# Kernel optimization log

Hardware: AMD Instinct MI355X
Metric: run time of the kernel (lower is better)

## Reference

```python
import jax, jax.numpy as jnp
import numpy as np

EMBED_NUM = 50000
EMBED_DIM = 300
HIDDEN = 512          # per-direction GRU hidden
ATT = 256             # attention_size
LABELS = 3
B, S = 64, 256
MAX_NORM = 5.0        # embedding max_norm


def _gru_dir(xw, Whh, bhh, hidden):
    """Run a single-direction GRU. xw: precomputed input proj [B,S,3H]."""
    def step(h, xt):
        gh = h @ Whh.T + bhh                      # [B,3H]
        xr, xz, xn = jnp.split(xt, 3, axis=-1)
        hr, hz, hn = jnp.split(gh, 3, axis=-1)
        r = jax.nn.sigmoid(xr + hr)
        z = jax.nn.sigmoid(xz + hz)
        n = jnp.tanh(xn + r * hn)
        h = (1.0 - z) * n + z * h
        return h, h
    h0 = jnp.zeros((xw.shape[0], hidden), dtype=xw.dtype)
    _, hs = jax.lax.scan(step, h0, jnp.swapaxes(xw, 0, 1))  # [S,B,H]
    return jnp.swapaxes(hs, 0, 1)                            # [B,S,H]


def setup_inputs() -> dict:
    key = jax.random.key(0)
    ks = jax.random.split(key, 20)
    x = jax.random.randint(ks[0], (B, S), 0, EMBED_NUM)
    target_start = jax.random.randint(ks[1], (B,), 0, S - 32)
    span = jax.random.randint(ks[2], (B,), 0, 20)
    target_end = jnp.minimum(target_start + span, S - 1)

    def rn(k, shape, fan_in):
        return jax.random.normal(k, shape, dtype=jnp.float32) * (1.0 / np.sqrt(fan_in))

    return {
        "x": x, "target_start": target_start, "target_end": target_end,
        "emb": jax.random.normal(ks[3], (EMBED_NUM, EMBED_DIM), dtype=jnp.float32) * 0.1,
        "Wih_f": rn(ks[4], (3 * HIDDEN, EMBED_DIM), EMBED_DIM),
        "Whh_f": rn(ks[5], (3 * HIDDEN, HIDDEN), HIDDEN),
        "bih_f": jnp.zeros((3 * HIDDEN,), jnp.float32),
        "bhh_f": jnp.zeros((3 * HIDDEN,), jnp.float32),
        "Wih_b": rn(ks[6], (3 * HIDDEN, EMBED_DIM), EMBED_DIM),
        "Whh_b": rn(ks[7], (3 * HIDDEN, HIDDEN), HIDDEN),
        "bih_b": jnp.zeros((3 * HIDDEN,), jnp.float32),
        "bhh_b": jnp.zeros((3 * HIDDEN,), jnp.float32),
        "W1": rn(ks[8], (ATT, 4 * HIDDEN), 4 * HIDDEN),
        "b1": jnp.zeros((ATT,), jnp.float32),
        "u": rn(ks[9], (ATT, ATT), ATT),
        "W2": rn(ks[10], (LABELS, 2 * HIDDEN), 2 * HIDDEN),
        "b2": jnp.zeros((LABELS,), jnp.float32),
    }


def reference(x, target_start, target_end, emb, Wih_f, Whh_f, bih_f, bhh_f,
              Wih_b, Whh_b, bih_b, bhh_b, W1, b1, u, W2, b2):
    # Embedding lookup with max_norm renorm (p=2), dropout = identity (eval)
    e = emb[x]                                                   # [B,S,E]
    nrm = jnp.linalg.norm(e, axis=-1, keepdims=True)
    e = e * jnp.minimum(1.0, MAX_NORM / (nrm + 1e-7))

    # Bidirectional GRU
    h_f = _gru_dir(e @ Wih_f.T + bih_f, Whh_f, bhh_f, HIDDEN)
    xb = e[:, ::-1, :]
    h_b = _gru_dir(xb @ Wih_b.T + bih_b, Whh_b, bhh_b, HIDDEN)[:, ::-1, :]
    h = jnp.concatenate([h_f, h_b], axis=-1)                     # [B,S,2H]

    # Ragged span mean-pool (vectorized replacement of the python loop)
    t = jnp.arange(S)
    mask = (t[None, :] >= target_start[:, None]) & (t[None, :] <= target_end[:, None])
    cnt = (target_end - target_start + 1).astype(h.dtype)        # [B]
    target = (h * mask[..., None].astype(h.dtype)).sum(axis=1) / cnt[:, None]  # [B,2H]

    # Concat each timestep hidden with its batch's target vector
    cat = jnp.concatenate([h, jnp.broadcast_to(target[:, None, :], h.shape)], axis=-1)  # [B,S,4H]
    o = jnp.tanh(cat @ W1.T + b1)                                # [B,S,A]

    # Per-batch attention scoring: beta[b] = u @ o[b]^T  -> [B,A,S]
    beta = jnp.einsum("ka,bsa->bks", u, o)
    alfa = jax.nn.softmax(beta, axis=-1)                         # softmax over sequence
    result = jnp.einsum("bks,bsh->bkh", alfa, h)                 # [B,A,2H]
    return result @ W2.T + b2                                    # [B,A,LABELS]
```

## Files before the change

### kernel.cpp

```cpp
#include <hip/hip_runtime.h>
#include <math.h>

#define BB   64
#define SS   256
#define ED   300
#define EDP  304
#define HH   512
#define G3   1536
#define ATT_ 256
#define BS_  16384
#define CHK  64
#define NCHK 4

__global__ void k_embed(const int* __restrict__ x, const float* __restrict__ emb,
                        float* __restrict__ e) {
    int row = blockIdx.x;
    int tok = x[row];
    const float* src = emb + (size_t)tok * ED;
    float* dst = e + (size_t)row * EDP;
    int tid = threadIdx.x;
    float v[3];
    float ss = 0.f;
#pragma unroll
    for (int i = 0; i < 3; ++i) {
        int k = tid + i * 128;
        float t = (k < ED) ? src[k] : 0.f;
        v[i] = t;
        ss += t * t;
    }
    for (int off = 32; off > 0; off >>= 1) ss += __shfl_xor(ss, off, 64);
    __shared__ float red[2];
    if ((tid & 63) == 0) red[tid >> 6] = ss;
    __syncthreads();
    float nrm = sqrtf(red[0] + red[1]);
    float scale = fminf(1.0f, 5.0f / (nrm + 1e-7f));
#pragma unroll
    for (int i = 0; i < 3; ++i) {
        int k = tid + i * 128;
        if (k < EDP) dst[k] = (k < ED) ? v[i] * scale : 0.f;
    }
}

#define PN0 933888
#define PN1 (PN0 + 3072)
#define PN2 (PN1 + 262144)
#define PN3 (PN2 + 1572864)

__global__ void k_prep_all(const float* __restrict__ Wihf, const float* __restrict__ Wihb,
                           const float* __restrict__ bihf, const float* __restrict__ bihb,
                           const float* __restrict__ W1,
                           const float* __restrict__ Whhf, const float* __restrict__ Whhb,
                           float* __restrict__ Wtc, float* __restrict__ bcc,
                           float* __restrict__ W1at, float* __restrict__ Wq) {
    int idx = blockIdx.x * blockDim.x + threadIdx.x;
    int stride = gridDim.x * blockDim.x;
    for (int i = idx; i < PN3; i += stride) {
        if (i < PN0) {
            int k = i / 3072, n = i - k * 3072;
            int dir = n >= 1536, nn = n - dir * 1536;
            const float* Wih = dir ? Wihb : Wihf;
            Wtc[i] = (k < ED) ? Wih[(size_t)nn * ED + k] : 0.f;
        } else if (i < PN1) {
            int j = i - PN0;
            bcc[j] = (j < 1536) ? bihf[j] : bihb[j - 1536];
        } else if (i < PN2) {
            int j = i - PN1;
            int n = j >> 10, k = j & 1023;
            W1at[(size_t)k * ATT_ + n] = W1[(size_t)n * 2048 + k];
        } else {
            int j = i - PN2;
            int dir = j / 786432, jj = j - dir * 786432;
            const float* Whh = dir ? Whhb : Whhf;
            int oc  = jj / 98304;
            int rem = jj - oc * 98304;
            int m   = rem / 3072;
            int r2  = rem - m * 3072;
            int t   = r2 >> 2;
            int e   = r2 & 3;
            int r   = t >> 2;
            int ks  = t & 3;
            int g   = r >> 6;
            int ul  = r & 63;
            int u   = oc * 64 + ul;
            int kq  = (oc * 16 + ks + 4 * m) & 127;
            Wq[j] = Whh[((size_t)(g * 512 + u)) * 512 + kq * 4 + e];
        }
    }
}

#define BSKEW(n) ((n) + (((n) >> 5) << 2))

template <int KT, int EPI>
__global__ void __launch_bounds__(256) k_gemm128(
    const float* __restrict__ A, int lda, long strideA,
    const float* __restrict__ Bm, int ldb, long strideB,
    float* __restrict__ C, int ldc, long strideC,
    int M, int N, int K,
    const float* __restrict__ bias, const float* __restrict__ bias2,
    int spos0, int spos1) {
    __shared__ float As[KT * 132];
    __shared__ float Bs[KT * 144];
    const int tid = threadIdx.x;
    const int tx = tid & 15, ty = tid >> 4;
    const int mbase = blockIdx.y * 128, nbase = blockIdx.x * 128;
    const int spos = (spos0 >= 0 && nbase >= 1536) ? spos1 : spos0;
    const float* Ab = A + (long)blockIdx.z * strideA;
    const float* Bb = Bm + (long)blockIdx.z * strideB;
    float* Cb = C + (long)blockIdx.z * strideC;
    float acc[8][8] = {};
    const int bgrp = tx * 8 + ((tx >> 2) << 2);
    for (int k0 = 0; k0 < K; k0 += KT) {
#pragma unroll
        for (int t = 0; t < 2; ++t) {
            int f = tid * 2 + t;
            int r = f >> 2, c4 = f & 3;
            int row = mbase + r;
            int arow = (spos >= 0) ? ((row >> 6) * 256 + spos + (row & 63)) : row;
            float4 a = *(const float4*)&Ab[(size_t)arow * lda + k0 + c4 * 4];
            As[(c4 * 4 + 0) * 132 + r] = a.x;
            As[(c4 * 4 + 1) * 132 + r] = a.y;
            As[(c4 * 4 + 2) * 132 + r] = a.z;
            As[(c4 * 4 + 3) * 132 + r] = a.w;
        }
#pragma unroll
        for (int t = 0; t < 2; ++t) {
            int f = tid * 2 + t;
            int kk = f >> 5, n = (f & 31) * 4;
            float4 b = *(const float4*)&Bb[(size_t)(k0 + kk) * ldb + nbase + n];
            *(float4*)&Bs[kk * 144 + BSKEW(n)] = b;
        }
        __syncthreads();
#pragma unroll
        for (int kk = 0; kk < KT; ++kk) {
            const float4* pa = (const float4*)&As[kk * 132 + ty * 8];
            float4 a0 = pa[0], a1 = pa[1];
            const float4* pb = (const float4*)&Bs[kk * 144 + bgrp];
            float4 b0 = pb[0], b1 = pb[1];
            float av[8] = {a0.x, a0.y, a0.z, a0.w, a1.x, a1.y, a1.z, a1.w};
            float bv[8] = {b0.x, b0.y, b0.z, b0.w, b1.x, b1.y, b1.z, b1.w};
#pragma unroll
            for (int i = 0; i < 8; ++i)
#pragma unroll
                for (int j = 0; j < 8; ++j) acc[i][j] += av[i] * bv[j];
        }
        __syncthreads();
    }
    if (EPI == 3) {
        const int row0 = mbase + ty * 8;
        const size_t bb = (size_t)(row0 >> 8) * strideC;
#pragma unroll
        for (int j = 0; j < 8; ++j) {
            int col = nbase + tx * 8 + j;
            float vj[8];
#pragma unroll
            for (int i = 0; i < 8; ++i) {
                int row = row0 + i;
                vj[i] = tanhf(acc[i][j] + bias2[(size_t)(row >> 8) * ATT_ + col]);
            }
            float* cp = &Cb[bb + (size_t)col * ldc + (row0 & 255)];
            ((float4*)cp)[0] = make_float4(vj[0], vj[1], vj[2], vj[3]);
            ((float4*)cp)[1] = make_float4(vj[4], vj[5], vj[6], vj[7]);
        }
    } else {
#pragma unroll
        for (int i = 0; i < 8; ++i) {
            int row = mbase + ty * 8 + i;
            float vout[8];
#pragma unroll
            for (int j = 0; j < 8; ++j) {
                int col = nbase + tx * 8 + j;
                float v = acc[i][j];
                if (EPI == 1) v += bias[col];
                if (EPI == 2) v = tanhf(v + bias2[(size_t)(row >> 8) * ATT_ + col]);
                vout[j] = v;
            }
            float4* cp = (float4*)&Cb[(size_t)row * ldc + nbase + tx * 8];
            cp[0] = make_float4(vout[0], vout[1], vout[2], vout[3]);
            cp[1] = make_float4(vout[4], vout[5], vout[6], vout[7]);
        }
    }
}

__device__ __forceinline__ float sigmoidf_(float v) { return 1.f / (1.f + expf(-v)); }

#define GRU_FMA4(mm)                                                        \
    {                                                                       \
        float4 h0 = hs4[kq];                                                \
        float4 h1 = hs4[128 + kq];                                          \
        float4 h2 = hs4[256 + kq];                                          \
        float4 h3 = hs4[384 + kq];                                          \
        float4 w = wp[(size_t)(mm) * 768];                                  \
        acc0 += h0.x * w.x + h0.y * w.y + h0.z * w.z + h0.w * w.w;          \
        acc1 += h1.x * w.x + h1.y * w.y + h1.z * w.z + h1.w * w.w;          \
        acc2 += h2.x * w.x + h2.y * w.y + h2.z * w.z + h2.w * w.w;          \
        acc3 += h3.x * w.x + h3.y * w.y + h3.z * w.z + h3.w * w.w;          \
        kq = (kq + 4) & 127;                                                \
    }

__global__ void __launch_bounds__(768)
k_gru_oct(const float* __restrict__ xw,
          const float* __restrict__ Wq,
          const float* __restrict__ bhhf, const float* __restrict__ bhhb,
          float* __restrict__ h_all,
          float* __restrict__ hx,
          unsigned* __restrict__ flg,
          int c) {
    const int bid   = blockIdx.x;
    const int group = bid >> 4;
    const int dir   = (bid >> 3) & 1;
    const int oc    = bid & 7;
    const int tid   = threadIdx.x;
    const float* __restrict__ bhh = dir ? bhhb : bhhf;
    const float4* __restrict__ wp =
        (const float4*)Wq + (size_t)(dir * 8 + oc) * 24576 + tid;
    __shared__ __align__(16) float hs[2048];
    __shared__ float gact[768];

    if (c == 0) {
        for (int t = tid; t < 2048; t += 768) hs[t] = 0.f;
    } else {
        const int prevpos = dir ? (256 - CHK * c) : (CHK * c - 1);
        for (int t = tid; t < 2048; t += 768) {
            int bb = t >> 9, uu = t & 511;
            hs[t] = h_all[((size_t)(group * 4 + bb) * 256 + prevpos) * 1024 +
                          dir * 512 + uu];
        }
    }
    const int ks  = tid & 3;
    const int r   = tid >> 2;
    const int bbg = tid >> 6;
    const int ulg = tid & 63;
    const int ug  = oc * 64 + ulg;
    float b0 = 0.f, b1 = 0.f, b2 = 0.f;
    if (tid < 256) { b0 = bhh[ug]; b1 = bhh[512 + ug]; b2 = bhh[1024 + ug]; }
    const int fbase = (dir * 16 + group) * 8;
    const int fi = (fbase + oc) * 32;
    __syncthreads();
    const float4* __restrict__ hs4 = (const float4*)hs;

    for (int j = 0; j < CHK; ++j) {
        const int gi  = c * CHK + j;
        const int pos = dir ? (255 - gi) : gi;
        float ph0 = 0.f, ph1 = 0.f, ph2 = 0.f;
        if (j > 0) {
            if (tid < 7) {
                const unsigned* f = &flg[(fbase + ((oc + 1 + tid) & 7)) * 32];
                while (__hip_atomic_load(f, __ATOMIC_RELAXED,
                                         __HIP_MEMORY_SCOPE_AGENT) < (unsigned)gi)
                    __builtin_amdgcn_s_sleep(1);
            }
            __syncthreads();
            const float* hxb = hx + (((size_t)((gi - 1) & 1) * 2 + dir) * 16 +
                                     group) * 2048;
            {
                int i0 = tid;
                int bb = i0 / 448, pi = i0 - bb * 448;
                int pu = pi + ((pi >= oc * 64) ? 64 : 0);
                ph0 = __hip_atomic_load(&hxb[bb * 512 + pu], __ATOMIC_RELAXED,
                                        __HIP_MEMORY_SCOPE_AGENT);
                int i1 = tid + 768;
                bb = i1 / 448; pi = i1 - bb * 448;
                pu = pi + ((pi >= oc * 64) ? 64 : 0);
                ph1 = __hip_atomic_load(&hxb[bb * 512 + pu], __ATOMIC_RELAXED,
                                        __HIP_MEMORY_SCOPE_AGENT);
                if (tid < 256) {
                    int i2 = tid + 1536;
                    bb = i2 / 448; pi = i2 - bb * 448;
                    pu = pi + ((pi >= oc * 64) ? 64 : 0);
                    ph2 = __hip_atomic_load(&hxb[bb * 512 + pu], __ATOMIC_RELAXED,
                                            __HIP_MEMORY_SCOPE_AGENT);
                }
            }
        }
        float xr = 0.f, xz = 0.f, xn = 0.f;
        if (tid < 256) {
            const int b = group * 4 + bbg;
            const int crow = b * CHK + (dir ? (CHK - 1 - j) : j);
            const float* __restrict__ xrow = xw + (size_t)crow * 3072 + dir * 1536;
            xr = xrow[ug]; xz = xrow[512 + ug]; xn = xrow[1024 + ug];
        }
        if (gi > 0) {
            float acc0 = 0.f, acc1 = 0.f, acc2 = 0.f, acc3 = 0.f;
            int kq = oc * 16 + ks;
            if (j > 0) {
#pragma unroll
                for (int m = 0; m < 4; ++m) GRU_FMA4(m);
                {
                    int i0 = tid;
                    int bb = i0 / 448, pi = i0 - bb * 448;
                    int pu = pi + ((pi >= oc * 64) ? 64 : 0);
                    hs[bb * 512 + pu] = ph0;
                    int i1 = tid + 768;
                    bb = i1 / 448; pi = i1 - bb * 448;
                    pu = pi + ((pi >= oc * 64) ? 64 : 0);
                    hs[bb * 512 + pu] = ph1;
                    if (tid < 256) {
                        int i2 = tid + 1536;
                        bb = i2 / 448; pi = i2 - bb * 448;
                        pu = pi + ((pi >= oc * 64) ? 64 : 0);
                        hs[bb * 512 + pu] = ph2;
                    }
                }
                __syncthreads();
#pragma unroll 4
                for (int m = 4; m < 32; ++m) GRU_FMA4(m);
            } else {
#pragma unroll 4
                for (int m = 0; m < 32; ++m) GRU_FMA4(m);
            }
            acc0 += __shfl_xor(acc0, 1, 64); acc0 += __shfl_xor(acc0, 2, 64);
            acc1 += __shfl_xor(acc1, 1, 64); acc1 += __shfl_xor(acc1, 2, 64);
            acc2 += __shfl_xor(acc2, 1, 64); acc2 += __shfl_xor(acc2, 2, 64);
            acc3 += __shfl_xor(acc3, 1, 64); acc3 += __shfl_xor(acc3, 2, 64);
            if (ks == 0) {
                gact[r] = acc0;
                gact[192 + r] = acc1;
                gact[384 + r] = acc2;
                gact[576 + r] = acc3;
            }
        }
        __syncthreads();
        if (tid < 256) {
            float hr = (gi > 0) ? gact[bbg * 192 + ulg] : 0.f;
            float hz = (gi > 0) ? gact[bbg * 192 + 64 + ulg] : 0.f;
            float hn = (gi > 0) ? gact[bbg * 192 + 128 + ulg] : 0.f;
            float rr = sigmoidf_(xr + b0 + hr);
            float zz = sigmoidf_(xz + b1 + hz);
            float nn = tanhf(xn + rr * (b2 + hn));
            float h = (1.f - zz) * nn + zz * hs[bbg * 512 + ug];
            hs[bbg * 512 + ug] = h;
            const int b = group * 4 + bbg;
            __hip_atomic_store(&h_all[((size_t)b * 256 + pos) * 1024 +
                                      dir * 512 + ug],
                               h, __ATOMIC_RELAXED, __HIP_MEMORY_SCOPE_AGENT);
            __hip_atomic_store(&hx[(((size_t)(gi & 1) * 2 + dir) * 16 + group) *
                                       2048 + bbg * 512 + ug],
                               h, __ATOMIC_RELAXED, __HIP_MEMORY_SCOPE_AGENT);
        }
        __syncthreads();
        if (tid == 0)
            __hip_atomic_store(&flg[fi], (unsigned)(gi + 1), __ATOMIC_RELEASE,
                               __HIP_MEMORY_SCOPE_AGENT);
    }
}

__global__ void k_target_tmp2(const float* __restrict__ h_all,
                              const int* __restrict__ ts, const int* __restrict__ te,
                              const float* __restrict__ W1, const float* __restrict__ b1,
                              float* __restrict__ tmp2) {
    int b = blockIdx.x;
    int tid = threadIdx.x;
    __shared__ __align__(16) float tg[1024];
    int s0 = ts[b], s1 = te[b];
    float inv = 1.f / (float)(s1 - s0 + 1);
    for (int d = tid; d < 1024; d += 256) {
        float acc = 0.f;
        for (int s = s0; s <= s1; ++s) acc += h_all[((size_t)b * 256 + s) * 1024 + d];
        tg[d] = acc * inv;
    }
    __syncthreads();
    const float4* wrow = (const float4*)(W1 + (size_t)tid * 2048 + 1024);
    const float4* tg4 = (const float4*)tg;
    float acc = b1[tid];
    for (int k = 0; k < 256; ++k) {
        float4 w = wrow[k], t = tg4[k];
        acc += w.x * t.x + w.y * t.y + w.z * t.z + w.w * t.w;
    }
    tmp2[(size_t)b * ATT_ + tid] = acc;
}

__global__ void k_softmax(float* __restrict__ beta) {
    int row = blockIdx.x;
    float* p = beta + (size_t)row * 256;
    int tid = threadIdx.x;
    float v = p[tid];
    float m = v;
    for (int off = 32; off > 0; off >>= 1) m = fmaxf(m, __shfl_xor(m, off, 64));
    __shared__ float red[4];
    if ((tid & 63) == 0) red[tid >> 6] = m;
    __syncthreads();
    m = fmaxf(fmaxf(red[0], red[1]), fmaxf(red[2], red[3]));
    float e = expf(v - m);
    float ssum = e;
    for (int off = 32; off > 0; off >>= 1) ssum += __shfl_xor(ssum, off, 64);
    __shared__ float red2[4];
    if ((tid & 63) == 0) red2[tid >> 6] = ssum;
    __syncthreads();
    float tot = red2[0] + red2[1] + red2[2] + red2[3];
    p[tid] = e / tot;
}

__global__ void k_final(const float* __restrict__ result, const float* __restrict__ W2,
                        const float* __restrict__ b2, float* __restrict__ out) {
    int row = blockIdx.x;
    int tid = threadIdx.x;
    const float* r = result + (size_t)row * 1024;
    float a0 = 0.f, a1 = 0.f, a2 = 0.f;
    for (int h = tid; h < 1024; h += 256) {
        float rv = r[h];
        a0 += rv * W2[h];
        a1 += rv * W2[1024 + h];
        a2 += rv * W2[2048 + h];
    }
    for (int off = 32; off > 0; off >>= 1) {
        a0 += __shfl_xor(a0, off, 64);
        a1 += __shfl_xor(a1, off, 64);
        a2 += __shfl_xor(a2, off, 64);
    }
    __shared__ float red[4][3];
    if ((tid & 63) == 0) {
        red[tid >> 6][0] = a0; red[tid >> 6][1] = a1; red[tid >> 6][2] = a2;
    }
    __syncthreads();
    if (tid < 3) {
        float s = red[0][tid] + red[1][tid] + red[2][tid] + red[3][tid];
        out[(size_t)row * 3 + tid] = s + b2[tid];
    }
}

extern "C" void kernel_launch(void* const* d_in, const int* in_sizes, int n_in,
                              void* d_out, int out_size, void* d_ws, size_t ws_size,
                              hipStream_t stream) {
    const int*   x      = (const int*)d_in[0];
    const int*   tstart = (const int*)d_in[1];
    const int*   tend   = (const int*)d_in[2];
    const float* emb    = (const float*)d_in[3];
    const float* Wihf   = (const float*)d_in[4];
    const float* Whhf   = (const float*)d_in[5];
    const float* bihf   = (const float*)d_in[6];
    const float* bhhf   = (const float*)d_in[7];
    const float* Wihb   = (const float*)d_in[8];
    const float* Whhb   = (const float*)d_in[9];
    const float* bihb   = (const float*)d_in[10];
    const float* bhhb   = (const float*)d_in[11];
    const float* W1     = (const float*)d_in[12];
    const float* b1     = (const float*)d_in[13];
    const float* u      = (const float*)d_in[14];
    const float* W2     = (const float*)d_in[15];
    const float* b2     = (const float*)d_in[16];
    float* out = (float*)d_out;
    float* ws = (float*)d_ws;

    float* h_p    = ws;
    float* e_p    = h_p + 16777216;
    float* xwc_p  = e_p + 4980736;
    float* Wq_p   = xwc_p + 12582912;
    float* Wtc_p  = Wq_p + 1572864;
    float* pad_p  = Wtc_p + 933888;
    float* bcc_p  = pad_p + 1700000;
    float* W1at_p = bcc_p + 3072;
    float* tg_p   = W1at_p + 262144;
    float* t2_p   = tg_p + 65536;
    float* beta_p = t2_p + 16384;
    float* hx_p   = beta_p + 4194304;
    unsigned* flg_p = (unsigned*)(hx_p + 131072);
    float* ot_p   = e_p;
    float* res_p  = xwc_p;

    if (ws_size < (size_t)43236512 * 4) return;

    hipMemsetAsync(flg_p, 0, 16384 * sizeof(unsigned), stream);
    k_embed<<<BS_, 128, 0, stream>>>(x, emb, e_p);
    k_prep_all<<<1024, 256, 0, stream>>>(Wihf, Wihb, bihf, bihb, W1, Whhf, Whhb,
                                         Wtc_p, bcc_p, W1at_p, Wq_p);
    for (int c = 0; c < NCHK; ++c) {
        k_gemm128<16, 1><<<dim3(24, 32, 1), 256, 0, stream>>>(
            e_p, EDP, 0, Wtc_p, 3072, 0, xwc_p, 3072, 0, BB * CHK, 3072, EDP,
            bcc_p, nullptr, CHK * c, 192 - CHK * c);
        k_gru_oct<<<256, 768, 0, stream>>>(xwc_p, Wq_p, bhhf, bhhb,
                                           h_p, hx_p, flg_p, c);
    }
    k_target_tmp2<<<BB, 256, 0, stream>>>(h_p, tstart, tend, W1, b1, t2_p);
    k_gemm128<16, 3><<<dim3(2, 128, 1), 256, 0, stream>>>(
        h_p, 1024, 0, W1at_p, ATT_, 0, ot_p, ATT_, 65536, BS_, ATT_, 1024,
        nullptr, t2_p, -1, -1);
    k_gemm128<16, 0><<<dim3(2, 2, BB), 256, 0, stream>>>(
        u, ATT_, 0, ot_p, ATT_, 65536, beta_p, ATT_, 65536, ATT_, ATT_, ATT_,
        nullptr, nullptr, -1, -1);
    k_softmax<<<BS_, 256, 0, stream>>>(beta_p);
    k_gemm128<16, 0><<<dim3(8, 2, BB), 256, 0, stream>>>(
        beta_p, ATT_, 65536, h_p, 1024, 262144, res_p, 1024, 262144,
        ATT_, 1024, ATT_, nullptr, nullptr, -1, -1);
    k_final<<<BS_, 256, 0, stream>>>(res_p, W2, b2, out);
}
```

Baseline: 3.683 ms.

## Split GRU recurrence across 16 blocks per batch group instead of 8

The persistent GRU kernel now splits each direction's 512 hidden units across 16 blocks of 384 threads instead of 8 blocks of 768, with 512 blocks in total. The recurrent weight layout and the flag handshake are reworked to match. Each block reloads the full hidden state from the exchange buffer, including its own slice, so the old skip-own-slice index math goes away. The aim is to spread the per-step matvec over more CUs and cut per-block latency. The cost is twice as many blocks polling flags and synchronising each step, and all 512 blocks must be co-resident for the spin-wait to avoid deadlock.

New measurement: 5.179 ms. 40.6% more time.

```diff
diff --git a/kernel.cpp b/kernel.cpp
--- a/kernel.cpp
+++ b/kernel.cpp
@@ -71,18 +71,18 @@
             int j = i - PN2;
             int dir = j / 786432, jj = j - dir * 786432;
             const float* Whh = dir ? Whhb : Whhf;
-            int oc  = jj / 98304;
-            int rem = jj - oc * 98304;
-            int m   = rem / 3072;
-            int r2  = rem - m * 3072;
+            int sp  = jj / 49152;
+            int rem = jj - sp * 49152;
+            int m   = rem / 1536;
+            int r2  = rem - m * 1536;
             int t   = r2 >> 2;
             int e   = r2 & 3;
             int r   = t >> 2;
             int ks  = t & 3;
-            int g   = r >> 6;
-            int ul  = r & 63;
-            int u   = oc * 64 + ul;
-            int kq  = (oc * 16 + ks + 4 * m) & 127;
+            int g   = r >> 5;
+            int ul  = r & 31;
+            int u   = sp * 32 + ul;
+            int kq  = (sp * 8 + ks + 4 * m) & 127;
             Wq[j] = Whh[((size_t)(g * 512 + u)) * 512 + kq * 4 + e];
         }
     }
@@ -189,7 +189,7 @@
         float4 h1 = hs4[128 + kq];                                          \
         float4 h2 = hs4[256 + kq];                                          \
         float4 h3 = hs4[384 + kq];                                          \
-        float4 w = wp[(size_t)(mm) * 768];                                  \
+        float4 w = wp[(size_t)(mm) * 384];                                  \
         acc0 += h0.x * w.x + h0.y * w.y + h0.z * w.z + h0.w * w.w;          \
         acc1 += h1.x * w.x + h1.y * w.y + h1.z * w.z + h1.w * w.w;          \
         acc2 += h2.x * w.x + h2.y * w.y + h2.z * w.z + h2.w * w.w;          \
@@ -197,8 +197,8 @@
         kq = (kq + 4) & 127;                                                \
     }
 
-__global__ void __launch_bounds__(768)
-k_gru_oct(const float* __restrict__ xw,
+__global__ void __launch_bounds__(384)
+k_gru_hex(const float* __restrict__ xw,
           const float* __restrict__ Wq,
           const float* __restrict__ bhhf, const float* __restrict__ bhhb,
           float* __restrict__ h_all,
@@ -206,21 +206,21 @@
           unsigned* __restrict__ flg,
           int c) {
     const int bid   = blockIdx.x;
-    const int group = bid >> 4;
-    const int dir   = (bid >> 3) & 1;
-    const int oc    = bid & 7;
+    const int group = bid >> 5;
+    const int dir   = (bid >> 4) & 1;
+    const int sp    = bid & 15;
     const int tid   = threadIdx.x;
     const float* __restrict__ bhh = dir ? bhhb : bhhf;
     const float4* __restrict__ wp =
-        (const float4*)Wq + (size_t)(dir * 8 + oc) * 24576 + tid;
+        (const float4*)Wq + (size_t)(dir * 16 + sp) * 12288 + tid;
     __shared__ __align__(16) float hs[2048];
-    __shared__ float gact[768];
+    __shared__ float gact[384];
 
     if (c == 0) {
-        for (int t = tid; t < 2048; t += 768) hs[t] = 0.f;
+        for (int t = tid; t < 2048; t += 384) hs[t] = 0.f;
     } else {
         const int prevpos = dir ? (256 - CHK * c) : (CHK * c - 1);
-        for (int t = tid; t < 2048; t += 768) {
+        for (int t = tid; t < 2048; t += 384) {
             int bb = t >> 9, uu = t & 511;
             hs[t] = h_all[((size_t)(group * 4 + bb) * 256 + prevpos) * 1024 +
                           dir * 512 + uu];
@@ -228,23 +228,23 @@
     }
     const int ks  = tid & 3;
     const int r   = tid >> 2;
-    const int bbg = tid >> 6;
-    const int ulg = tid & 63;
-    const int ug  = oc * 64 + ulg;
+    const int bbg = tid >> 5;
+    const int ulg = tid & 31;
+    const int ug  = sp * 32 + ulg;
     float b0 = 0.f, b1 = 0.f, b2 = 0.f;
-    if (tid < 256) { b0 = bhh[ug]; b1 = bhh[512 + ug]; b2 = bhh[1024 + ug]; }
-    const int fbase = (dir * 16 + group) * 8;
-    const int fi = (fbase + oc) * 32;
+    if (tid < 128) { b0 = bhh[ug]; b1 = bhh[512 + ug]; b2 = bhh[1024 + ug]; }
+    const int fbase = (dir * 16 + group) * 16;
+    const int fi = (fbase + sp) * 32;
     __syncthreads();
     const float4* __restrict__ hs4 = (const float4*)hs;
 
     for (int j = 0; j < CHK; ++j) {
         const int gi  = c * CHK + j;
         const int pos = dir ? (255 - gi) : gi;
-        float ph0 = 0.f, ph1 = 0.f, ph2 = 0.f;
+        float ph0 = 0.f, ph1 = 0.f, ph2 = 0.f, ph3 = 0.f, ph4 = 0.f, ph5 = 0.f;
         if (j > 0) {
-            if (tid < 7) {
-                const unsigned* f = &flg[(fbase + ((oc + 1 + tid) & 7)) * 32];
+            if (tid < 15) {
+                const unsigned* f = &flg[(fbase + ((sp + 1 + tid) & 15)) * 32];
                 while (__hip_atomic_load(f, __ATOMIC_RELAXED,
                                          __HIP_MEMORY_SCOPE_AGENT) < (unsigned)gi)
                     __builtin_amdgcn_s_sleep(1);
@@ -252,28 +252,22 @@
             __syncthreads();
             const float* hxb = hx + (((size_t)((gi - 1) & 1) * 2 + dir) * 16 +
                                      group) * 2048;
-            {
-                int i0 = tid;
-                int bb = i0 / 448, pi = i0 - bb * 448;
-                int pu = pi + ((pi >= oc * 64) ? 64 : 0);
-                ph0 = __hip_atomic_load(&hxb[bb * 512 + pu], __ATOMIC_RELAXED,
+            ph0 = __hip_atomic_load(&hxb[tid], __ATOMIC_RELAXED,
+                                    __HIP_MEMORY_SCOPE_AGENT);
+            ph1 = __hip_atomic_load(&hxb[tid + 384], __ATOMIC_RELAXED,
+                                    __HIP_MEMORY_SCOPE_AGENT);
+            ph2 = __hip_atomic_load(&hxb[tid + 768], __ATOMIC_RELAXED,
+                                    __HIP_MEMORY_SCOPE_AGENT);
+            ph3 = __hip_atomic_load(&hxb[tid + 1152], __ATOMIC_RELAXED,
+                                    __HIP_MEMORY_SCOPE_AGENT);
+            ph4 = __hip_atomic_load(&hxb[tid + 1536], __ATOMIC_RELAXED,
+                                    __HIP_MEMORY_SCOPE_AGENT);
+            if (tid < 128)
+                ph5 = __hip_atomic_load(&hxb[tid + 1920], __ATOMIC_RELAXED,
                                         __HIP_MEMORY_SCOPE_AGENT);
-                int i1 = tid + 768;
-                bb = i1 / 448; pi = i1 - bb * 448;
-                pu = pi + ((pi >= oc * 64) ? 64 : 0);
-                ph1 = __hip_atomic_load(&hxb[bb * 512 + pu], __ATOMIC_RELAXED,
-                                        __HIP_MEMORY_SCOPE_AGENT);
-                if (tid < 256) {
-                    int i2 = tid + 1536;
-                    bb = i2 / 448; pi = i2 - bb * 448;
-                    pu = pi + ((pi >= oc * 64) ? 64 : 0);
-                    ph2 = __hip_atomic_load(&hxb[bb * 512 + pu], __ATOMIC_RELAXED,
-                                            __HIP_MEMORY_SCOPE_AGENT);
-                }
-            }
         }
         float xr = 0.f, xz = 0.f, xn = 0.f;
-        if (tid < 256) {
+        if (tid < 128) {
             const int b = group * 4 + bbg;
             const int crow = b * CHK + (dir ? (CHK - 1 - j) : j);
             const float* __restrict__ xrow = xw + (size_t)crow * 3072 + dir * 1536;
@@ -281,29 +275,18 @@
         }
         if (gi > 0) {
             float acc0 = 0.f, acc1 = 0.f, acc2 = 0.f, acc3 = 0.f;
-            int kq = oc * 16 + ks;
+            int kq = sp * 8 + ks;
             if (j > 0) {
-#pragma unroll
-                for (int m = 0; m < 4; ++m) GRU_FMA4(m);
-                {
-                    int i0 = tid;
-                    int bb = i0 / 448, pi = i0 - bb * 448;
-                    int pu = pi + ((pi >= oc * 64) ? 64 : 0);
-                    hs[bb * 512 + pu] = ph0;
-                    int i1 = tid + 768;
-                    bb = i1 / 448; pi = i1 - bb * 448;
-                    pu = pi + ((pi >= oc * 64) ? 64 : 0);
-                    hs[bb * 512 + pu] = ph1;
-                    if (tid < 256) {
-                        int i2 = tid + 1536;
-                        bb = i2 / 448; pi = i2 - bb * 448;
-                        pu = pi + ((pi >= oc * 64) ? 64 : 0);
-                        hs[bb * 512 + pu] = ph2;
-                    }
-                }
+                GRU_FMA4(0); GRU_FMA4(1);
+                hs[tid] = ph0;
+                hs[tid + 384] = ph1;
+                hs[tid + 768] = ph2;
+                hs[tid + 1152] = ph3;
+                hs[tid + 1536] = ph4;
+                if (tid < 128) hs[tid + 1920] = ph5;
                 __syncthreads();
-#pragma unroll 4
-                for (int m = 4; m < 32; ++m) GRU_FMA4(m);
+#pragma unroll 5
+                for (int m = 2; m < 32; ++m) GRU_FMA4(m);
             } else {
 #pragma unroll 4
                 for (int m = 0; m < 32; ++m) GRU_FMA4(m);
@@ -314,16 +297,16 @@
             acc3 += __shfl_xor(acc3, 1, 64); acc3 += __shfl_xor(acc3, 2, 64);
             if (ks == 0) {
                 gact[r] = acc0;
-                gact[192 + r] = acc1;
-                gact[384 + r] = acc2;
-                gact[576 + r] = acc3;
+                gact[96 + r] = acc1;
+                gact[192 + r] = acc2;
+                gact[288 + r] = acc3;
             }
         }
         __syncthreads();
-        if (tid < 256) {
-            float hr = (gi > 0) ? gact[bbg * 192 + ulg] : 0.f;
-            float hz = (gi > 0) ? gact[bbg * 192 + 64 + ulg] : 0.f;
-            float hn = (gi > 0) ? gact[bbg * 192 + 128 + ulg] : 0.f;
+        if (tid < 128) {
+            float hr = (gi > 0) ? gact[bbg * 96 + ulg] : 0.f;
+            float hz = (gi > 0) ? gact[bbg * 96 + 32 + ulg] : 0.f;
+            float hn = (gi > 0) ? gact[bbg * 96 + 64 + ulg] : 0.f;
             float rr = sigmoidf_(xr + b0 + hr);
             float zz = sigmoidf_(xz + b1 + hz);
             float nn = tanhf(xn + rr * (b2 + hn));
@@ -467,7 +450,7 @@
         k_gemm128<16, 1><<<dim3(24, 32, 1), 256, 0, stream>>>(
             e_p, EDP, 0, Wtc_p, 3072, 0, xwc_p, 3072, 0, BB * CHK, 3072, EDP,
             bcc_p, nullptr, CHK * c, 192 - CHK * c);
-        k_gru_oct<<<256, 768, 0, stream>>>(xwc_p, Wq_p, bhhf, bhhb,
+        k_gru_hex<<<512, 384, 0, stream>>>(xwc_p, Wq_p, bhhf, bhhb,
                                            h_p, hx_p, flg_p, c);
     }
     k_target_tmp2<<<BB, 256, 0, stream>>>(h_p, tstart, tend, W1, b1, t2_p);
```

## Keep GRU recurrent weights in registers and fuse gate reduction per thread

Applied to the files above, without the earlier changes.

The recurrent GRU kernel now loads each block's slice of Whh (48 float4 per thread) into registers once per launch instead of streaming weights from global memory every timestep. Threads are remapped so each of 512 threads owns one hidden unit across all three gates, reducing across 8 k-slices with shuffles. This removes the shared-memory gate buffer and the per-step weight reads, and the weight prep permutation is changed to match. The cost is heavy register pressure (192 VGPRs for weights alone) and an epilogue where only 1/8 of threads compute gate activations for all 4 batch rows.

New measurement: 9.690 ms. +163.1%, slower.

```diff
diff --git a/kernel.cpp b/kernel.cpp
--- a/kernel.cpp
+++ b/kernel.cpp
@@ -39,6 +39,11 @@
         int k = tid + i * 128;
         if (k < EDP) dst[k] = (k < ED) ? v[i] * scale : 0.f;
     }
+}
+
+__host__ __device__ __forceinline__ int kq_of(int oc, int ks, int m) {
+    return (m < 2) ? (oc * 16 + 2 * ks + m)
+                   : ((oc * 16 + 16 + ks * 14 + (m - 2)) & 127);
 }
 
 #define PN0 933888
@@ -73,17 +78,16 @@
             const float* Whh = dir ? Whhb : Whhf;
             int oc  = jj / 98304;
             int rem = jj - oc * 98304;
-            int m   = rem / 3072;
-            int r2  = rem - m * 3072;
-            int t   = r2 >> 2;
-            int e   = r2 & 3;
-            int r   = t >> 2;
-            int ks  = t & 3;
-            int g   = r >> 6;
-            int ul  = r & 63;
-            int u   = oc * 64 + ul;
-            int kq  = (oc * 16 + ks + 4 * m) & 127;
-            Wq[j] = Whh[((size_t)(g * 512 + u)) * 512 + kq * 4 + e];
+            int m   = rem / 6144;
+            int r3  = rem - m * 6144;
+            int g   = r3 / 2048;
+            int r4  = r3 - g * 2048;
+            int t   = r4 >> 2;
+            int e   = r4 & 3;
+            int u   = t >> 3;
+            int ks  = t & 7;
+            int kq  = kq_of(oc, ks, m);
+            Wq[j] = Whh[((size_t)(g * 512 + oc * 64 + u)) * 512 + kq * 4 + e];
         }
     }
 }
@@ -183,22 +187,31 @@
 
 __device__ __forceinline__ float sigmoidf_(float v) { return 1.f / (1.f + expf(-v)); }
 
-#define GRU_FMA4(mm)                                                        \
+#define RFMA(mm, kv)                                                        \
     {                                                                       \
-        float4 h0 = hs4[kq];                                                \
-        float4 h1 = hs4[128 + kq];                                          \
-        float4 h2 = hs4[256 + kq];                                          \
-        float4 h3 = hs4[384 + kq];                                          \
-        float4 w = wp[(size_t)(mm) * 768];                                  \
-        acc0 += h0.x * w.x + h0.y * w.y + h0.z * w.z + h0.w * w.w;          \
-        acc1 += h1.x * w.x + h1.y * w.y + h1.z * w.z + h1.w * w.w;          \
-        acc2 += h2.x * w.x + h2.y * w.y + h2.z * w.z + h2.w * w.w;          \
-        acc3 += h3.x * w.x + h3.y * w.y + h3.z * w.z + h3.w * w.w;          \
-        kq = (kq + 4) & 127;                                                \
-    }
-
-__global__ void __launch_bounds__(768)
-k_gru_oct(const float* __restrict__ xw,
+        float4 h0 = hs4[kv];                                                \
+        float4 h1 = hs4[128 + (kv)];                                        \
+        float4 h2 = hs4[256 + (kv)];                                        \
+        float4 h3 = hs4[384 + (kv)];                                        \
+        float4 w = wreg[(mm) * 3 + 0];                                      \
+        a0[0] += h0.x*w.x + h0.y*w.y + h0.z*w.z + h0.w*w.w;                 \
+        a0[1] += h1.x*w.x + h1.y*w.y + h1.z*w.z + h1.w*w.w;                 \
+        a0[2] += h2.x*w.x + h2.y*w.y + h2.z*w.z + h2.w*w.w;                 \
+        a0[3] += h3.x*w.x + h3.y*w.y + h3.z*w.z + h3.w*w.w;                 \
+        w = wreg[(mm) * 3 + 1];                                             \
+        a1[0] += h0.x*w.x + h0.y*w.y + h0.z*w.z + h0.w*w.w;                 \
+        a1[1] += h1.x*w.x + h1.y*w.y + h1.z*w.z + h1.w*w.w;                 \
+        a1[2] += h2.x*w.x + h2.y*w.y + h2.z*w.z + h2.w*w.w;                 \
+        a1[3] += h3.x*w.x + h3.y*w.y + h3.z*w.z + h3.w*w.w;                 \
+        w = wreg[(mm) * 3 + 2];                                             \
+        a2[0] += h0.x*w.x + h0.y*w.y + h0.z*w.z + h0.w*w.w;                 \
+        a2[1] += h1.x*w.x + h1.y*w.y + h1.z*w.z + h1.w*w.w;                 \
+        a2[2] += h2.x*w.x + h2.y*w.y + h2.z*w.z + h2.w*w.w;                 \
+        a2[3] += h3.x*w.x + h3.y*w.y + h3.z*w.z + h3.w*w.w;                 \
+    }
+
+__global__ void __launch_bounds__(512)
+k_gru_reg(const float* __restrict__ xw,
           const float* __restrict__ Wq,
           const float* __restrict__ bhhf, const float* __restrict__ bhhb,
           float* __restrict__ h_all,
@@ -210,29 +223,30 @@
     const int dir   = (bid >> 3) & 1;
     const int oc    = bid & 7;
     const int tid   = threadIdx.x;
+    const int u     = tid >> 3;
+    const int ks    = tid & 7;
+    const int ug    = oc * 64 + u;
     const float* __restrict__ bhh = dir ? bhhb : bhhf;
+    __shared__ __align__(16) float hs[2048];
+
     const float4* __restrict__ wp =
         (const float4*)Wq + (size_t)(dir * 8 + oc) * 24576 + tid;
-    __shared__ __align__(16) float hs[2048];
-    __shared__ float gact[768];
+    float4 wreg[48];
+#pragma unroll
+    for (int i = 0; i < 48; ++i) wreg[i] = wp[(size_t)i * 512];
 
     if (c == 0) {
-        for (int t = tid; t < 2048; t += 768) hs[t] = 0.f;
+        for (int t = tid; t < 2048; t += 512) hs[t] = 0.f;
     } else {
         const int prevpos = dir ? (256 - CHK * c) : (CHK * c - 1);
-        for (int t = tid; t < 2048; t += 768) {
+        for (int t = tid; t < 2048; t += 512) {
             int bb = t >> 9, uu = t & 511;
             hs[t] = h_all[((size_t)(group * 4 + bb) * 256 + prevpos) * 1024 +
                           dir * 512 + uu];
         }
     }
-    const int ks  = tid & 3;
-    const int r   = tid >> 2;
-    const int bbg = tid >> 6;
-    const int ulg = tid & 63;
-    const int ug  = oc * 64 + ulg;
     float b0 = 0.f, b1 = 0.f, b2 = 0.f;
-    if (tid < 256) { b0 = bhh[ug]; b1 = bhh[512 + ug]; b2 = bhh[1024 + ug]; }
+    if (ks == 0) { b0 = bhh[ug]; b1 = bhh[512 + ug]; b2 = bhh[1024 + ug]; }
     const int fbase = (dir * 16 + group) * 8;
     const int fi = (fbase + oc) * 32;
     __syncthreads();
@@ -241,7 +255,7 @@
     for (int j = 0; j < CHK; ++j) {
         const int gi  = c * CHK + j;
         const int pos = dir ? (255 - gi) : gi;
-        float ph0 = 0.f, ph1 = 0.f, ph2 = 0.f;
+        float ph0 = 0.f, ph1 = 0.f, ph2 = 0.f, ph3 = 0.f;
         if (j > 0) {
             if (tid < 7) {
                 const unsigned* f = &flg[(fbase + ((oc + 1 + tid) & 7)) * 32];
@@ -258,84 +272,97 @@
                 int pu = pi + ((pi >= oc * 64) ? 64 : 0);
                 ph0 = __hip_atomic_load(&hxb[bb * 512 + pu], __ATOMIC_RELAXED,
                                         __HIP_MEMORY_SCOPE_AGENT);
-                int i1 = tid + 768;
+                int i1 = tid + 512;
                 bb = i1 / 448; pi = i1 - bb * 448;
                 pu = pi + ((pi >= oc * 64) ? 64 : 0);
                 ph1 = __hip_atomic_load(&hxb[bb * 512 + pu], __ATOMIC_RELAXED,
                                         __HIP_MEMORY_SCOPE_AGENT);
+                int i2 = tid + 1024;
+                bb = i2 / 448; pi = i2 - bb * 448;
+                pu = pi + ((pi >= oc * 64) ? 64 : 0);
+                ph2 = __hip_atomic_load(&hxb[bb * 512 + pu], __ATOMIC_RELAXED,
+                                        __HIP_MEMORY_SCOPE_AGENT);
                 if (tid < 256) {
-                    int i2 = tid + 1536;
-                    bb = i2 / 448; pi = i2 - bb * 448;
+                    int i3 = tid + 1536;
+                    bb = i3 / 448; pi = i3 - bb * 448;
                     pu = pi + ((pi >= oc * 64) ? 64 : 0);
-                    ph2 = __hip_atomic_load(&hxb[bb * 512 + pu], __ATOMIC_RELAXED,
+                    ph3 = __hip_atomic_load(&hxb[bb * 512 + pu], __ATOMIC_RELAXED,
                                             __HIP_MEMORY_SCOPE_AGENT);
                 }
             }
         }
-        float xr = 0.f, xz = 0.f, xn = 0.f;
-        if (tid < 256) {
-            const int b = group * 4 + bbg;
-            const int crow = b * CHK + (dir ? (CHK - 1 - j) : j);
-            const float* __restrict__ xrow = xw + (size_t)crow * 3072 + dir * 1536;
-            xr = xrow[ug]; xz = xrow[512 + ug]; xn = xrow[1024 + ug];
-        }
+        float a0[4] = {0.f, 0.f, 0.f, 0.f};
+        float a1[4] = {0.f, 0.f, 0.f, 0.f};
+        float a2[4] = {0.f, 0.f, 0.f, 0.f};
         if (gi > 0) {
-            float acc0 = 0.f, acc1 = 0.f, acc2 = 0.f, acc3 = 0.f;
-            int kq = oc * 16 + ks;
             if (j > 0) {
-#pragma unroll
-                for (int m = 0; m < 4; ++m) GRU_FMA4(m);
+                RFMA(0, oc * 16 + 2 * ks);
+                RFMA(1, oc * 16 + 2 * ks + 1);
                 {
                     int i0 = tid;
                     int bb = i0 / 448, pi = i0 - bb * 448;
                     int pu = pi + ((pi >= oc * 64) ? 64 : 0);
                     hs[bb * 512 + pu] = ph0;
-                    int i1 = tid + 768;
+                    int i1 = tid + 512;
                     bb = i1 / 448; pi = i1 - bb * 448;
                     pu = pi + ((pi >= oc * 64) ? 64 : 0);
                     hs[bb * 512 + pu] = ph1;
+                    int i2 = tid + 1024;
+                    bb = i2 / 448; pi = i2 - bb * 448;
+                    pu = pi + ((pi >= oc * 64) ? 64 : 0);
+                    hs[bb * 512 + pu] = ph2;
                     if (tid < 256) {
-                        int i2 = tid + 1536;
-                        bb = i2 / 448; pi = i2 - bb * 448;
+                        int i3 = tid + 1536;
+                        bb = i3 / 448; pi = i3 - bb * 448;
                         pu = pi + ((pi >= oc * 64) ? 64 : 0);
-                        hs[bb * 512 + pu] = ph2;
+                        hs[bb * 512 + pu] = ph3;
                     }
                 }
                 __syncthreads();
-#pragma unroll 4
-                for (int m = 4; m < 32; ++m) GRU_FMA4(m);
+                int kq = (oc * 16 + 16 + ks * 14) & 127;
+#pragma unroll
+                for (int m = 2; m < 16; ++m) { RFMA(m, kq); kq = (kq + 1) & 127; }
             } else {
-#pragma unroll 4
-                for (int m = 0; m < 32; ++m) GRU_FMA4(m);
-            }
-            acc0 += __shfl_xor(acc0, 1, 64); acc0 += __shfl_xor(acc0, 2, 64);
-            acc1 += __shfl_xor(acc1, 1, 64); acc1 += __shfl_xor(acc1, 2, 64);
-            acc2 += __shfl_xor(acc2, 1, 64); acc2 += __shfl_xor(acc2, 2, 64);
-            acc3 += __shfl_xor(acc3, 1, 64); acc3 += __shfl_xor(acc3, 2, 64);
-            if (ks == 0) {
-                gact[r] = acc0;
-                gact[192 + r] = acc1;
-                gact[384 + r] = acc2;
-                gact[576 + r] = acc3;
+                RFMA(0, oc * 16 + 2 * ks);
+                RFMA(1, oc * 16 + 2 * ks + 1);
+                int kq = (oc * 16 + 16 + ks * 14) & 127;
+#pragma unroll
+                for (int m = 2; m < 16; ++m) { RFMA(m, kq); kq = (kq + 1) & 127; }
+            }
+#pragma unroll
+            for (int bb = 0; bb < 4; ++bb) {
+                a0[bb] += __shfl_xor(a0[bb], 1, 64);
+                a0[bb] += __shfl_xor(a0[bb], 2, 64);
+                a0[bb] += __shfl_xor(a0[bb], 4, 64);
+                a1[bb] += __shfl_xor(a1[bb], 1, 64);
+                a1[bb] += __shfl_xor(a1[bb], 2, 64);
+                a1[bb] += __shfl_xor(a1[bb], 4, 64);
+                a2[bb] += __shfl_xor(a2[bb], 1, 64);
+                a2[bb] += __shfl_xor(a2[bb], 2, 64);
+                a2[bb] += __shfl_xor(a2[bb], 4, 64);
             }
         }
         __syncthreads();
-        if (tid < 256) {
-            float hr = (gi > 0) ? gact[bbg * 192 + ulg] : 0.f;
-            float hz = (gi > 0) ? gact[bbg * 192 + 64 + ulg] : 0.f;
-            float hn = (gi > 0) ? gact[bbg * 192 + 128 + ulg] : 0.f;
-            float rr = sigmoidf_(xr + b0 + hr);
-            float zz = sigmoidf_(xz + b1 + hz);
-            float nn = tanhf(xn + rr * (b2 + hn));
-            float h = (1.f - zz) * nn + zz * hs[bbg * 512 + ug];
-            hs[bbg * 512 + ug] = h;
-            const int b = group * 4 + bbg;
-            __hip_atomic_store(&h_all[((size_t)b * 256 + pos) * 1024 +
-                                      dir * 512 + ug],
-                               h, __ATOMIC_RELAXED, __HIP_MEMORY_SCOPE_AGENT);
-            __hip_atomic_store(&hx[(((size_t)(gi & 1) * 2 + dir) * 16 + group) *
-                                       2048 + bbg * 512 + ug],
-                               h, __ATOMIC_RELAXED, __HIP_MEMORY_SCOPE_AGENT);
+        if (ks == 0) {
+#pragma unroll
+            for (int bb = 0; bb < 4; ++bb) {
+                const int b = group * 4 + bb;
+                const int crow = b * CHK + (dir ? (CHK - 1 - j) : j);
+                const float* __restrict__ xrow =
+                    xw + (size_t)crow * 3072 + dir * 1536;
+                float xr = xrow[ug], xz = xrow[512 + ug], xn = xrow[1024 + ug];
+                float rr = sigmoidf_(xr + b0 + a0[bb]);
+                float zz = sigmoidf_(xz + b1 + a1[bb]);
+                float nn = tanhf(xn + rr * (b2 + a2[bb]));
+                float h = (1.f - zz) * nn + zz * hs[bb * 512 + ug];
+                hs[bb * 512 + ug] = h;
+                __hip_atomic_store(&h_all[((size_t)b * 256 + pos) * 1024 +
+                                          dir * 512 + ug],
+                                   h, __ATOMIC_RELAXED, __HIP_MEMORY_SCOPE_AGENT);
+                __hip_atomic_store(&hx[(((size_t)(gi & 1) * 2 + dir) * 16 +
+                                        group) * 2048 + bb * 512 + ug],
+                                   h, __ATOMIC_RELAXED, __HIP_MEMORY_SCOPE_AGENT);
+            }
         }
         __syncthreads();
         if (tid == 0)
@@ -467,7 +494,7 @@
         k_gemm128<16, 1><<<dim3(24, 32, 1), 256, 0, stream>>>(
             e_p, EDP, 0, Wtc_p, 3072, 0, xwc_p, 3072, 0, BB * CHK, 3072, EDP,
             bcc_p, nullptr, CHK * c, 192 - CHK * c);
-        k_gru_oct<<<256, 768, 0, stream>>>(xwc_p, Wq_p, bhhf, bhhb,
+        k_gru_reg<<<256, 512, 0, stream>>>(xwc_p, Wq_p, bhhf, bhhb,
                                            h_p, hx_p, flg_p, c);
     }
     k_target_tmp2<<<BB, 256, 0, stream>>>(h_p, tstart, tend, W1, b1, t2_p);
```
